# Performance work log

Measured on AMD Instinct MI355X. Metric: run time of the kernel, lower is better.

Reference implementation:

```python
import jax, jax.numpy as jnp
import numpy as np

B, NV, DM, DK, DV, H, DFF = 256, 40, 512, 256, 256, 4, 2048
K1, K2 = 4, 8
EPS = 1e-5


def _knn_mask(vertices, k):
    # square_distance(xyz, xyz): dist[b,i,j] = ||x_i - x_j||^2
    d = -2.0 * jnp.einsum('bic,bjc->bij', vertices, vertices)
    sq = jnp.sum(vertices ** 2, -1)
    d = d + sq[:, :, None] + sq[:, None, :]
    # torch.topk(dist, k, dim=1, largest=False)[1].transpose(1,2) -> [B,N,k]
    idx = jax.lax.top_k(-jnp.swapaxes(d, 1, 2), k)[1]
    counts = jax.nn.one_hot(idx, NV, dtype=jnp.float32).sum(-2)  # [B,N,NV]
    return (counts < 1.0)[:, None, :, :]  # [B,1,N,N], broadcasts over heads (== repeat)


def _ln(x, g, b):
    m = x.mean(-1, keepdims=True)
    v = x.var(-1, keepdims=True)
    return (x - m) / jnp.sqrt(v + EPS) * g + b


def _encoder(x, mask, wq, bq, wk, bk, wv, bv, wo, bo, ln1g, ln1b, w1, b1, w2, b2, ln2g, ln2b):
    Bn, N, _ = x.shape
    q = (x @ wq + bq).reshape(Bn, N, H, DK).transpose(0, 2, 1, 3)   # [B,H,N,DK]
    kk = (x @ wk + bk).reshape(Bn, N, H, DK).transpose(0, 2, 3, 1)  # [B,H,DK,N]
    v = (x @ wv + bv).reshape(Bn, N, H, DV).transpose(0, 2, 1, 3)   # [B,H,N,DV]
    att = jnp.matmul(q, kk) / np.sqrt(DK)                           # [B,H,N,N]
    att = jnp.where(mask, -jnp.inf, att)
    att = jax.nn.softmax(att, axis=-1)
    o = jnp.matmul(att, v).transpose(0, 2, 1, 3).reshape(Bn, N, H * DV) @ wo + bo
    x = _ln(x + o, ln1g, ln1b)                                      # residual + LayerNorm
    ff = jax.nn.relu(x @ w1 + b1) @ w2 + b2                         # position-wise FFN
    return _ln(x + ff, ln2g, ln2b)


def _fusion(y, w1, b1, bng, bnb, w2, b2):
    y = y @ w1 + b1                       # Conv1d(1024,512,1) == per-position linear
    m = y.mean((0, 1))
    v = y.var((0, 1))                     # BatchNorm1d, training-mode batch stats (biased var)
    y = (y - m) / jnp.sqrt(v + EPS) * bng + bnb
    y = jnp.where(y > 0, y, 0.2 * y)      # LeakyReLU(0.2)
    return y @ w2 + b2                    # Conv1d(512,512,1)


def _forward(vertices, F, *p):
    m1 = _knn_mask(vertices, K1)
    m2 = _knn_mask(vertices, K2)
    F1 = _encoder(F, m1, *p[0:16])
    F2 = _encoder(F, m2, *p[16:32])
    yy = jnp.concatenate((F1, F2), -1)    # [B,N,2*DM]
    return _fusion(yy, *p[32:38])


def setup_inputs() -> dict:
    key = jax.random.key(0)
    d = {}
    cnt = [0]
    def nk():
        cnt[0] += 1
        return jax.random.fold_in(key, cnt[0])
    def lin(i, o):
        return jax.random.normal(nk(), (i, o), jnp.float32) * (1.0 / np.sqrt(i))
    d['vertices'] = jax.random.normal(nk(), (B, NV, 3), jnp.float32)
    d['F'] = jax.random.normal(nk(), (B, NV, DM), jnp.float32)
    for pfx in ('e1', 'e2'):
        d[pfx + '_wq'] = lin(DM, H * DK); d[pfx + '_bq'] = jnp.zeros((H * DK,), jnp.float32)
        d[pfx + '_wk'] = lin(DM, H * DK); d[pfx + '_bk'] = jnp.zeros((H * DK,), jnp.float32)
        d[pfx + '_wv'] = lin(DM, H * DV); d[pfx + '_bv'] = jnp.zeros((H * DV,), jnp.float32)
        d[pfx + '_wo'] = lin(H * DV, DM); d[pfx + '_bo'] = jnp.zeros((DM,), jnp.float32)
        d[pfx + '_ln1g'] = jnp.ones((DM,), jnp.float32); d[pfx + '_ln1b'] = jnp.zeros((DM,), jnp.float32)
        d[pfx + '_w1'] = lin(DM, DFF); d[pfx + '_b1'] = jnp.zeros((DFF,), jnp.float32)
        d[pfx + '_w2'] = lin(DFF, DM); d[pfx + '_b2'] = jnp.zeros((DM,), jnp.float32)
        d[pfx + '_ln2g'] = jnp.ones((DM,), jnp.float32); d[pfx + '_ln2b'] = jnp.zeros((DM,), jnp.float32)
    d['fus_w1'] = lin(2 * DM, DM); d['fus_b1'] = jnp.zeros((DM,), jnp.float32)
    d['fus_bng'] = jnp.ones((DM,), jnp.float32); d['fus_bnb'] = jnp.zeros((DM,), jnp.float32)
    d['fus_w2'] = lin(DM, DM); d['fus_b2'] = jnp.zeros((DM,), jnp.float32)
    return d


def reference(vertices, F,
              e1_wq, e1_bq, e1_wk, e1_bk, e1_wv, e1_bv, e1_wo, e1_bo,
              e1_ln1g, e1_ln1b, e1_w1, e1_b1, e1_w2, e1_b2, e1_ln2g, e1_ln2b,
              e2_wq, e2_bq, e2_wk, e2_bk, e2_wv, e2_bv, e2_wo, e2_bo,
              e2_ln1g, e2_ln1b, e2_w1, e2_b1, e2_w2, e2_b2, e2_ln2g, e2_ln2b,
              fus_w1, fus_b1, fus_bng, fus_bnb, fus_w2, fus_b2):
    return _forward(vertices, F,
                    e1_wq, e1_bq, e1_wk, e1_bk, e1_wv, e1_bv, e1_wo, e1_bo,
                    e1_ln1g, e1_ln1b, e1_w1, e1_b1, e1_w2, e1_b2, e1_ln2g, e1_ln2b,
                    e2_wq, e2_bq, e2_wk, e2_bk, e2_wv, e2_bv, e2_wo, e2_bo,
                    e2_ln1g, e2_ln1b, e2_w1, e2_b1, e2_w2, e2_b2, e2_ln2g, e2_ln2b,
                    fus_w1, fus_b1, fus_bng, fus_bnb, fus_w2, fus_b2)
```

## Files before the change

### kernel.cpp

```cpp
#include <hip/hip_runtime.h>

typedef unsigned short u16;
typedef unsigned int   u32;
typedef __attribute__((ext_vector_type(4))) float f32x4;
typedef __attribute__((ext_vector_type(8))) short short8;
typedef __attribute__((ext_vector_type(4))) unsigned short u16x4;

#define DEV __device__ __forceinline__
#define AS1 __attribute__((address_space(1)))
#define AS3 __attribute__((address_space(3)))
#define SB  __builtin_amdgcn_sched_barrier(0)
#define BAR __builtin_amdgcn_s_barrier()

DEV float bf2f(u16 u){ return __uint_as_float(((u32)u)<<16); }
DEV u16 f2bf(float f){ u32 u=__float_as_uint(f); return (u16)((u + 0x7fffu + ((u>>16)&1u))>>16); }
DEV void g2lds16(const void* g, void* l){
  __builtin_amdgcn_global_load_lds((const AS1 void*)g, (AS3 void*)l, 16, 0, 0);
}

struct WtJobs {
  const float* W[14];
  u16*         WT[14];
  int K[14];
  int N[14];
  int off[15];
};

__global__ __launch_bounds__(256) void wtb_kernel(WtJobs J){
  __shared__ u16 tile[32][33];
  int bid = blockIdx.x;
  int j = 0;
  #pragma unroll
  for (int s=1;s<14;++s) if (bid >= J.off[s]) j = s;
  int lb = bid - J.off[j];
  int K = J.K[j], N = J.N[j];
  int nx = N>>5;
  int n0 = (lb % nx)<<5, k0 = (lb / nx)<<5;
  const float* W = J.W[j];
  u16* WT = J.WT[j];
  int tx = threadIdx.x, ty = threadIdx.y;
  #pragma unroll
  for (int i=0;i<4;++i){
    int k = ty + i*8;
    tile[k][tx] = f2bf(W[(size_t)(k0+k)*N + n0 + tx]);
  }
  __syncthreads();
  #pragma unroll
  for (int i=0;i<4;++i){
    int n = ty + i*8;
    WT[(size_t)(n0+n)*K + k0 + tx] = tile[tx][n];
  }
}

__global__ __launch_bounds__(256) void cvt_kernel(const float* __restrict__ in,
                                                  u16* __restrict__ out, long n4){
  long i = ((long)blockIdx.x*256 + threadIdx.x);
  if (i < n4){
    f32x4 v = *(const f32x4*)(in + i*4);
    u16x4 r; r.x=f2bf(v.x); r.y=f2bf(v.y); r.z=f2bf(v.z); r.w=f2bf(v.w);
    *(u16x4*)(out + i*4) = r;
  }
}

__global__ __launch_bounds__(256) void catb_kernel(const float* __restrict__ a,
                                                   const float* __restrict__ b,
                                                   const float* __restrict__ c,
                                                   float* __restrict__ dst){
  int i = blockIdx.x*256 + threadIdx.x;
  if (i < 1024) dst[i] = a[i];
  else if (i < 2048) dst[i] = b[i-1024];
  else if (i < 3072) dst[i] = c[i-2048];
}

__global__ __launch_bounds__(256) void fill_kernel(float* p, float v, long n){
  long i = (long)blockIdx.x*256 + threadIdx.x;
  if (i < n) p[i] = v;
}

__global__ __launch_bounds__(256) void knn_kernel(const float* __restrict__ verts,
                                                  unsigned char* __restrict__ nbr1,
                                                  unsigned char* __restrict__ nbr2){
  __shared__ float P[40][3];
  __shared__ float SQ[40];
  int b = blockIdx.x, tid = threadIdx.x, wave = tid>>6, lane = tid&63;
  if (tid < 40){
    float x = verts[((size_t)b*40+tid)*3+0];
    float y = verts[((size_t)b*40+tid)*3+1];
    float z = verts[((size_t)b*40+tid)*3+2];
    P[tid][0]=x; P[tid][1]=y; P[tid][2]=z;
    SQ[tid] = __fadd_rn(__fadd_rn(__fmul_rn(x,x),__fmul_rn(y,y)),__fmul_rn(z,z));
  }
  __syncthreads();
  for (int i = wave; i < 40; i += 4){
    float d = 3.0e38f;
    if (lane < 40){
      int j = lane;
      float dot = __fadd_rn(__fadd_rn(__fmul_rn(P[i][0],P[j][0]),
                                      __fmul_rn(P[i][1],P[j][1])),
                            __fmul_rn(P[i][2],P[j][2]));
      d = __fadd_rn(__fadd_rn(__fmul_rn(-2.f,dot), SQ[j]), SQ[i]);
    }
    bool taken = false;
    #pragma unroll
    for (int s=0;s<8;++s){
      float v = taken ? 3.0e38f : d;
      float m = v;
      #pragma unroll
      for (int o=32;o;o>>=1) m = fminf(m, __shfl_xor(m, o));
      unsigned long long mask = __ballot(v == m);
      int bj = __ffsll((unsigned long long)mask) - 1;
      if (lane == bj) taken = true;
      if (lane == 0){
        if (s < 4) nbr1[((size_t)b*40+i)*4+s] = (unsigned char)bj;
        nbr2[((size_t)b*40+i)*8+s] = (unsigned char)bj;
      }
    }
  }
}

template<int RELU, int OUTBF>
__global__ __launch_bounds__(256, 4) void gemm_bt(const u16* __restrict__ A,
                                                  const u16* __restrict__ BT,
                                                  const float* __restrict__ bias,
                                                  void* __restrict__ Cout,
                                                  int M, int N, int K){
  __shared__ u16 As[128*32];
  __shared__ u16 Bs[128*32];
  const int tid  = threadIdx.x;
  const int wave = tid>>6, lane = tid&63;
  const int wr = (wave>>1)<<6, wc = (wave&1)<<6;
  const int row0 = blockIdx.x<<7, col0 = blockIdx.y<<7;
  f32x4 acc[4][4];
  #pragma unroll
  for (int i=0;i<4;++i)
    #pragma unroll
    for (int j=0;j<4;++j) acc[i][j] = (f32x4){0.f,0.f,0.f,0.f};

  const int rL = lane>>2;
  const int ch = lane&3;
  const int fr = lane&15, fc = lane>>4;
  const short8* Asv = (const short8*)As;
  const short8* Bsv = (const short8*)Bs;

  for (int kt=0; kt<K; kt+=32){
    #pragma unroll
    for (int c=0;c<2;++c){
      int lo = c*4096 + wave*1024;
      int r  = c*64 + wave*16 + rL;
      int kk = ((ch ^ ((r>>1)&3))<<3);
      g2lds16(A  + (size_t)(row0+r)*K + kt + kk, (char*)As + lo);
      g2lds16(BT + (size_t)(col0+r)*K + kt + kk, (char*)Bs + lo);
    }
    __syncthreads();
    short8 a[4], b[4];
    #pragma unroll
    for (int i=0;i<4;++i){
      int rowA = wr + i*16 + fr;
      int rowB = wc + i*16 + fr;
      a[i] = Asv[rowA*4 + (fc ^ ((rowA>>1)&3))];
      b[i] = Bsv[rowB*4 + (fc ^ ((rowB>>1)&3))];
    }
    #pragma unroll
    for (int i=0;i<4;++i)
      #pragma unroll
      for (int j=0;j<4;++j)
        acc[i][j] = __builtin_amdgcn_mfma_f32_16x16x32_bf16(a[i], b[j], acc[i][j], 0,0,0);
    __syncthreads();
  }
  #pragma unroll
  for (int i=0;i<4;++i){
    int mrow = row0 + wr + i*16 + fc*4;
    #pragma unroll
    for (int j=0;j<4;++j){
      int ncol = col0 + wc + j*16 + fr;
      float bv = bias[ncol];
      #pragma unroll
      for (int r=0;r<4;++r){
        float v = acc[i][j][r] + bv;
        if (RELU) v = v > 0.f ? v : 0.f;
        if (OUTBF) ((u16*)Cout)[(size_t)(mrow+r)*N + ncol] = f2bf(v);
        else       ((float*)Cout)[(size_t)(mrow+r)*N + ncol] = v;
      }
    }
  }
}

DEV void stage32(const u16* __restrict__ gbase, int ldg, u16* __restrict__ buf,
                 int kt, int wave, int lane){
  int srw = wave*16 + (lane>>2);
  int scl = (lane&3) ^ ((srw>>1)&3);
  const u16* src = gbase + (size_t)srw*ldg + kt + scl*8;
  char* dst = (char*)buf + wave*1024;
  g2lds16(src, dst);
  g2lds16(src + (size_t)128*ldg, dst + 8192);
}

template<int RELU>
__global__ __launch_bounds__(512, 1) void gemm256p(const u16* __restrict__ A,
                                                   const u16* __restrict__ BT,
                                                   const float* __restrict__ bias,
                                                   u16* __restrict__ Cout,
                                                   int M, int N, int K){
  __shared__ u16 As[4][256*32];
  __shared__ u16 Bs[4][256*32];
  const int tid  = threadIdx.x;
  const int wave = tid>>6, lane = tid&63;
  const int wm = wave>>2, wn = wave&3;
  const int fr = lane&15, fc = lane>>4;
  const int row0 = blockIdx.x<<8, col0 = blockIdx.y<<8;
  const int NT = K>>5;
  const u16* Ag = A  + (size_t)row0*K;
  const u16* Bg = BT + (size_t)col0*K;

  f32x4 acc[8][4];
  #pragma unroll
  for (int i=0;i<8;++i)
    #pragma unroll
    for (int j=0;j<4;++j) acc[i][j] = (f32x4){0.f,0.f,0.f,0.f};

  stage32(Ag, K, As[0], 0,  wave, lane);  stage32(Bg, K, Bs[0], 0,  wave, lane);
  stage32(Ag, K, As[1], 32, wave, lane);  stage32(Bg, K, Bs[1], 32, wave, lane);
  stage32(Ag, K, As[2], 64, wave, lane);  stage32(Bg, K, Bs[2], 64, wave, lane);
  asm volatile("s_waitcnt vmcnt(8)" ::: "memory");
  SB; BAR; SB;

  for (int t = 0; t < NT; ++t){
    const int cur = t&3, nx3 = (t+3)&3;
    const short8* AV = (const short8*)As[cur];
    const short8* BV = (const short8*)Bs[cur];
    short8 a[4], b[4];
    #pragma unroll
    for (int nf=0;nf<4;++nf){ int rr = wn*64 + nf*16 + fr; b[nf] = BV[rr*4 + (fc ^ ((rr>>1)&3))]; }
    #pragma unroll
    for (int mf=0;mf<4;++mf){ int rr = wm*128 + mf*16 + fr; a[mf] = AV[rr*4 + (fc ^ ((rr>>1)&3))]; }
    if (t+3 < NT) stage32(Ag, K, As[nx3], (t+3)<<5, wave, lane);
    SB; BAR; SB;
    __builtin_amdgcn_s_setprio(1);
    #pragma unroll
    for (int mf=0;mf<4;++mf)
      #pragma unroll
      for (int nf=0;nf<4;++nf)
        acc[mf][nf] = __builtin_amdgcn_mfma_f32_16x16x32_bf16(a[mf], b[nf], acc[mf][nf], 0,0,0);
    __builtin_amdgcn_s_setprio(0);
    SB; BAR; SB;
    #pragma unroll
    for (int mf=0;mf<4;++mf){ int rr = wm*128 + (mf+4)*16 + fr; a[mf] = AV[rr*4 + (fc ^ ((rr>>1)&3))]; }
    if (t+3 < NT) stage32(Bg, K, Bs[nx3], (t+3)<<5, wave, lane);
    {
      int rem = NT - t - 1;
      if (rem >= 3)      asm volatile("s_waitcnt vmcnt(8)" ::: "memory");
      else if (rem == 2) asm volatile("s_waitcnt vmcnt(4)" ::: "memory");
      else if (rem == 1) asm volatile("s_waitcnt vmcnt(0)" ::: "memory");
    }
    SB; BAR; SB;
    __builtin_amdgcn_s_setprio(1);
    #pragma unroll
    for (int mf=0;mf<4;++mf)
      #pragma unroll
      for (int nf=0;nf<4;++nf)
        acc[mf+4][nf] = __builtin_amdgcn_mfma_f32_16x16x32_bf16(a[mf], b[nf], acc[mf+4][nf], 0,0,0);
    __builtin_amdgcn_s_setprio(0);
    SB; BAR; SB;
  }

  #pragma unroll
  for (int i=0;i<8;++i){
    int mrow = row0 + wm*128 + i*16 + fc*4;
    #pragma unroll
    for (int j=0;j<4;++j){
      int ncol = col0 + wn*64 + j*16 + fr;
      float bv = bias[ncol];
      #pragma unroll
      for (int r=0;r<4;++r){
        float v = acc[i][j][r] + bv;
        if (RELU) v = v > 0.f ? v : 0.f;
        Cout[(size_t)(mrow+r)*N + ncol] = f2bf(v);
      }
    }
  }
}

template<int KNB>
__global__ __launch_bounds__(256) void attn_kernel(const u16* __restrict__ QKV,
                                                   const unsigned char* __restrict__ nbr,
                                                   u16* __restrict__ O){
  __shared__ u16 KV[2][40*256];
  int b = blockIdx.x>>2, h = blockIdx.x&3;
  int tid = threadIdx.x, wave = tid>>6, lane = tid&63;
  const size_t rowb = (size_t)b*40;
  for (int c = tid; c < 1280; c += 256){
    int row = c >> 5, col = (c & 31) << 3;
    size_t src = (rowb+row)*3072 + h*256 + col;
    *(short8*)&KV[0][row*256+col] = *(const short8*)(QKV + src + 1024);
    *(short8*)&KV[1][row*256+col] = *(const short8*)(QKV + src + 2048);
  }
  __syncthreads();
  for (int i = wave; i < 40; i += 4){
    int js[KNB];
    if (KNB == 4){
      u32 p = *(const u32*)(nbr + (rowb+i)*4);
      js[0]=p&255; js[1]=(p>>8)&255; js[2]=(p>>16)&255; js[3]=(p>>24)&255;
    } else {
      u32 p0 = *(const u32*)(nbr + (rowb+i)*8);
      u32 p1 = *(const u32*)(nbr + (rowb+i)*8 + 4);
      js[0]=p0&255; js[1]=(p0>>8)&255; js[2]=(p0>>16)&255; js[3]=(p0>>24)&255;
      js[4]=p1&255; js[5]=(p1>>8)&255; js[6]=(p1>>16)&255; js[7]=(p1>>24)&255;
    }
    u16x4 qv = *(const u16x4*)(QKV + (rowb+i)*3072 + h*256 + lane*4);
    float q0=bf2f(qv.x), q1=bf2f(qv.y), q2=bf2f(qv.z), q3=bf2f(qv.w);
    float s[KNB];
    #pragma unroll
    for (int jj=0;jj<KNB;++jj){
      u16x4 kv = *(const u16x4*)&KV[0][js[jj]*256 + lane*4];
      s[jj] = q0*bf2f(kv.x) + q1*bf2f(kv.y) + q2*bf2f(kv.z) + q3*bf2f(kv.w);
    }
    #pragma unroll
    for (int jj=0;jj<KNB;++jj){
      #pragma unroll
      for (int o=32;o;o>>=1) s[jj] += __shfl_xor(s[jj], o);
      s[jj] *= 0.0625f;
    }
    float m = s[0];
    #pragma unroll
    for (int jj=1;jj<KNB;++jj) m = fmaxf(m, s[jj]);
    float sum = 0.f;
    #pragma unroll
    for (int jj=0;jj<KNB;++jj){ s[jj] = expf(s[jj]-m); sum += s[jj]; }
    float inv = 1.f/sum;
    float o0=0.f,o1=0.f,o2=0.f,o3=0.f;
    #pragma unroll
    for (int jj=0;jj<KNB;++jj){
      float w = s[jj]*inv;
      u16x4 vv = *(const u16x4*)&KV[1][js[jj]*256 + lane*4];
      o0 += w*bf2f(vv.x); o1 += w*bf2f(vv.y); o2 += w*bf2f(vv.z); o3 += w*bf2f(vv.w);
    }
    u16x4 r; r.x=f2bf(o0); r.y=f2bf(o1); r.z=f2bf(o2); r.w=f2bf(o3);
    *(u16x4*)(O + (rowb+i)*1024 + h*256 + lane*4) = r;
  }
}

DEV float blockReduce(float v, float* red){
  #pragma unroll
  for (int o=32;o;o>>=1) v += __shfl_xor(v, o);
  int lane = threadIdx.x&63, w = threadIdx.x>>6;
  if (lane==0) red[w] = v;
  __syncthreads();
  float t = red[0]+red[1]+red[2]+red[3];
  __syncthreads();
  return t;
}

__global__ __launch_bounds__(256) void ln_kernel(const float* __restrict__ resf,
                                                 const float* __restrict__ delta,
                                                 const float* __restrict__ g,
                                                 const float* __restrict__ be,
                                                 u16* __restrict__ outb, int ostride, int ocol,
                                                 float* __restrict__ outf){
  __shared__ float red[4];
  int row = blockIdx.x, tid = threadIdx.x;
  size_t ib = (size_t)row*512 + tid*2;
  float2 xr = *(const float2*)(resf+ib);
  float2 xd = *(const float2*)(delta+ib);
  float x0 = xr.x+xd.x, x1 = xr.y+xd.y;
  float s = blockReduce(x0+x1, red);
  float mean = s*(1.f/512.f);
  float d0 = x0-mean, d1 = x1-mean;
  float q = blockReduce(d0*d0+d1*d1, red);
  float inv = 1.f/sqrtf(q*(1.f/512.f)+1e-5f);
  float2 gg = *(const float2*)(g+tid*2);
  float2 bb = *(const float2*)(be+tid*2);
  float r0 = d0*inv*gg.x + bb.x;
  float r1 = d1*inv*gg.y + bb.y;
  size_t ob = (size_t)row*ostride + ocol + tid*2;
  *(u32*)(outb+ob) = ((u32)f2bf(r1)<<16) | (u32)f2bf(r0);
  if (outf){ *(float2*)(outf + ib) = make_float2(r0,r1); }
}

__global__ __launch_bounds__(512) void bn_part(const float* __restrict__ y,
                                               float* __restrict__ psum, float* __restrict__ psq){
  int c = threadIdx.x, blk = blockIdx.x;
  float s = 0.f, q = 0.f;
  for (int r = blk; r < 10240; r += 64){
    float v = y[(size_t)r*512 + c];
    s += v; q += v*v;
  }
  psum[blk*512+c] = s; psq[blk*512+c] = q;
}

__global__ __launch_bounds__(512) void bn_fin(const float* __restrict__ psum,
                                              const float* __restrict__ psq,
                                              const float* __restrict__ g,
                                              const float* __restrict__ b,
                                              float* __restrict__ scale, float* __restrict__ shift){
  int c = threadIdx.x;
  float s = 0.f, q = 0.f;
  for (int k=0;k<64;++k){ s += psum[k*512+c]; q += psq[k*512+c]; }
  float m = s*(1.f/10240.f);
  float var = q*(1.f/10240.f) - m*m;
  float sc = g[c]/sqrtf(var + 1e-5f);
  scale[c] = sc; shift[c] = b[c] - m*sc;
}

__global__ __launch_bounds__(256) void bn_apply(const float* __restrict__ y,
                                                const float* __restrict__ scale,
                                                const float* __restrict__ shift,
                                                u16* __restrict__ out){
  long i4 = ((long)blockIdx.x*256 + threadIdx.x)*4;
  if (i4 < (long)10240*512){
    int c = (int)(i4 & 511);
    f32x4 v  = *(const f32x4*)(y+i4);
    f32x4 sc = *(const f32x4*)(scale+c);
    f32x4 sh = *(const f32x4*)(shift+c);
    f32x4 r;
    #pragma unroll
    for (int k=0;k<4;++k){
      float t = v[k]*sc[k] + sh[k];
      r[k] = t > 0.f ? t : 0.2f*t;
    }
    u16x4 o; o.x=f2bf(r[0]); o.y=f2bf(r[1]); o.z=f2bf(r[2]); o.w=f2bf(r[3]);
    *(u16x4*)(out+i4) = o;
  }
}

extern "C" void kernel_launch(void* const* d_in, const int* in_sizes, int n_in,
                              void* d_out, int out_size, void* d_ws, size_t ws_size,
                              hipStream_t stream){
  const float* verts = (const float*)d_in[0];
  const float* F     = (const float*)d_in[1];
  const float* ew[2][16];
  for (int e=0;e<2;++e) for (int i=0;i<16;++i) ew[e][i] = (const float*)d_in[2+e*16+i];
  const float* fus_w1  = (const float*)d_in[34];
  const float* fus_b1  = (const float*)d_in[35];
  const float* fus_bng = (const float*)d_in[36];
  const float* fus_bnb = (const float*)d_in[37];
  const float* fus_w2  = (const float*)d_in[38];
  const float* fus_b2  = (const float*)d_in[39];

  const int M = 10240;
  size_t off = 0;
  auto alloc = [&](size_t bytes)->void*{
    void* p = (char*)d_ws + off; off = (off + bytes + 255) & ~(size_t)255; return p;
  };
  u16 *wtqkv[2],*wto[2],*wtw1[2],*wtw2[2];
  float* bqkv[2];
  for (int e=0;e<2;++e){
    wtqkv[e] = (u16*)alloc((size_t)3072*512*2);
    wto[e]   = (u16*)alloc((size_t)512*1024*2);
    wtw1[e]  = (u16*)alloc((size_t)2048*512*2);
    wtw2[e]  = (u16*)alloc((size_t)512*2048*2);
    bqkv[e]  = (float*)alloc(3072*4);
  }
  u16*  wtf1 = (u16*)alloc((size_t)512*1024*2);
  u16*  wtf2 = (u16*)alloc((size_t)512*512*2);
  u16*  Fb   = (u16*)alloc((size_t)M*512*2);
  u16*  QKVb = (u16*)alloc((size_t)M*3072*2);
  u16*  H1   = (u16*)alloc((size_t)M*2048*2);
  float* PF  = (float*)alloc((size_t)M*512*4);
  u16*  X1b  = (u16*)alloc((size_t)M*512*2);
  u16*  YC   = (u16*)alloc((size_t)M*1024*2);
  unsigned char* nbr1 = (unsigned char*)alloc(256*40*4);
  unsigned char* nbr2 = (unsigned char*)alloc(256*40*8);
  float* psum = (float*)alloc(64*512*4);
  float* psq  = (float*)alloc(64*512*4);
  float* bnsc = (float*)alloc(512*4);
  float* bnsh = (float*)alloc(512*4);
  u16*   OB  = H1;
  float* X1f = (float*)QKVb;
  float* Y1  = (float*)QKVb;
  u16*   Y2  = (u16*)((char*)QKVb + (size_t)M*512*4);

  if (off > ws_size){
    long n = out_size;
    fill_kernel<<<(unsigned)((n+255)/256),256,0,stream>>>((float*)d_out, 12345.0f, n);
    return;
  }

  WtJobs J;
  int nb = 0, ji = 0;
  auto addjob = [&](const float* W, u16* WT, int K, int N){
    J.W[ji]=W; J.WT[ji]=WT; J.K[ji]=K; J.N[ji]=N; J.off[ji]=nb;
    nb += (N>>5)*(K>>5); ++ji;
  };
  for (int e=0;e<2;++e){
    addjob(ew[e][0],  wtqkv[e],                    512, 1024);
    addjob(ew[e][2],  wtqkv[e]+(size_t)1024*512,   512, 1024);
    addjob(ew[e][4],  wtqkv[e]+(size_t)2048*512,   512, 1024);
    addjob(ew[e][6],  wto[e],  1024, 512);
    addjob(ew[e][10], wtw1[e], 512, 2048);
    addjob(ew[e][12], wtw2[e], 2048, 512);
  }
  addjob(fus_w1, wtf1, 1024, 512);
  addjob(fus_w2, wtf2, 512, 512);
  J.off[14] = nb;
  wtb_kernel<<<nb, dim3(32,8), 0, stream>>>(J);
  for (int e=0;e<2;++e)
    catb_kernel<<<12,256,0,stream>>>(ew[e][1], ew[e][3], ew[e][5], bqkv[e]);
  cvt_kernel<<<5120,256,0,stream>>>(F, Fb, (long)M*512/4);
  knn_kernel<<<256,256,0,stream>>>(verts, nbr1, nbr2);

  for (int e=0;e<2;++e){
    gemm256p<0><<<dim3(40,12),512,0,stream>>>(Fb, wtqkv[e], bqkv[e], QKVb, M, 3072, 512);
    if (e == 0) attn_kernel<4><<<1024,256,0,stream>>>(QKVb, nbr1, OB);
    else        attn_kernel<8><<<1024,256,0,stream>>>(QKVb, nbr2, OB);
    gemm_bt<0,0><<<dim3(80,4),256,0,stream>>>(OB, wto[e], ew[e][7], PF, M, 512, 1024);
    ln_kernel<<<M,256,0,stream>>>(F, PF, ew[e][8], ew[e][9], X1b, 512, 0, X1f);
    gemm256p<1><<<dim3(40,8),512,0,stream>>>(X1b, wtw1[e], ew[e][11], H1, M, 2048, 512);
    gemm_bt<0,0><<<dim3(80,4),256,0,stream>>>(H1, wtw2[e], ew[e][13], PF, M, 512, 2048);
    ln_kernel<<<M,256,0,stream>>>(X1f, PF, ew[e][14], ew[e][15], YC, 1024, e*512, nullptr);
  }

  gemm_bt<0,0><<<dim3(80,4),256,0,stream>>>(YC, wtf1, fus_b1, Y1, M, 512, 1024);
  bn_part<<<64,512,0,stream>>>(Y1, psum, psq);
  bn_fin<<<1,512,0,stream>>>(psum, psq, fus_bng, fus_bnb, bnsc, bnsh);
  bn_apply<<<5120,256,0,stream>>>(Y1, bnsc, bnsh, Y2);
  gemm_bt<0,0><<<dim3(80,4),256,0,stream>>>(Y2, wtf2, fus_b2, d_out, M, 512, 512);
}
```

Baseline: 551.9 us.

## Batch both encoders' post-attention GEMMs and LayerNorms via grid-z dispatch

Runs the QKV GEMM and attention for both encoders first, then processes the O-projection, LN1, FFN1, FFN2 and LN2 of both encoders together in single launches, using blockIdx.z (or y for LN) to select per-encoder pointers with strided layouts. The small 320-block gemm_bt launches become 640 blocks and the FFN1 GEMM grid doubles, which improves GPU fill and halves launch count. Intermediate projection outputs are now stored as bf16 instead of fp32, cutting memory traffic at some precision cost. BatchNorm partial reduction uses 256 blocks instead of 64 for more parallelism. Workspace grows because H1, PF and X1b are widened to hold both encoders.

```diff
diff --git a/kernel.cpp b/kernel.cpp
--- a/kernel.cpp
+++ b/kernel.cpp
@@ -118,12 +118,12 @@
   }
 }
 
+struct GemmZ { const u16* A; const u16* BT; const float* bias; void* C; };
+
 template<int RELU, int OUTBF>
-__global__ __launch_bounds__(256, 4) void gemm_bt(const u16* __restrict__ A,
-                                                  const u16* __restrict__ BT,
-                                                  const float* __restrict__ bias,
-                                                  void* __restrict__ Cout,
-                                                  int M, int N, int K){
+__global__ __launch_bounds__(256, 4) void gemm_btz(GemmZ g0, GemmZ g1,
+                                                   int M, int N, int K, int lda, int ldc){
+  GemmZ g = blockIdx.z ? g1 : g0;
   __shared__ u16 As[128*32];
   __shared__ u16 Bs[128*32];
   const int tid  = threadIdx.x;
@@ -148,8 +148,8 @@
       int lo = c*4096 + wave*1024;
       int r  = c*64 + wave*16 + rL;
       int kk = ((ch ^ ((r>>1)&3))<<3);
-      g2lds16(A  + (size_t)(row0+r)*K + kt + kk, (char*)As + lo);
-      g2lds16(BT + (size_t)(col0+r)*K + kt + kk, (char*)Bs + lo);
+      g2lds16(g.A  + (size_t)(row0+r)*lda + kt + kk, (char*)As + lo);
+      g2lds16(g.BT + (size_t)(col0+r)*K   + kt + kk, (char*)Bs + lo);
     }
     __syncthreads();
     short8 a[4], b[4];
@@ -173,13 +173,13 @@
     #pragma unroll
     for (int j=0;j<4;++j){
       int ncol = col0 + wc + j*16 + fr;
-      float bv = bias[ncol];
+      float bv = g.bias[ncol];
       #pragma unroll
       for (int r=0;r<4;++r){
         float v = acc[i][j][r] + bv;
         if (RELU) v = v > 0.f ? v : 0.f;
-        if (OUTBF) ((u16*)Cout)[(size_t)(mrow+r)*N + ncol] = f2bf(v);
-        else       ((float*)Cout)[(size_t)(mrow+r)*N + ncol] = v;
+        if (OUTBF) ((u16*)g.C)[(size_t)(mrow+r)*ldc + ncol] = f2bf(v);
+        else       ((float*)g.C)[(size_t)(mrow+r)*ldc + ncol] = v;
       }
     }
   }
@@ -196,11 +196,9 @@
 }
 
 template<int RELU>
-__global__ __launch_bounds__(512, 1) void gemm256p(const u16* __restrict__ A,
-                                                   const u16* __restrict__ BT,
-                                                   const float* __restrict__ bias,
-                                                   u16* __restrict__ Cout,
-                                                   int M, int N, int K){
+__global__ __launch_bounds__(512, 1) void gemm256pz(GemmZ g0, GemmZ g1,
+                                                    int M, int N, int K, int lda, int ldc){
+  GemmZ g = blockIdx.z ? g1 : g0;
   __shared__ u16 As[4][256*32];
   __shared__ u16 Bs[4][256*32];
   const int tid  = threadIdx.x;
@@ -209,8 +207,8 @@
   const int fr = lane&15, fc = lane>>4;
   const int row0 = blockIdx.x<<8, col0 = blockIdx.y<<8;
   const int NT = K>>5;
-  const u16* Ag = A  + (size_t)row0*K;
-  const u16* Bg = BT + (size_t)col0*K;
+  const u16* Ag = g.A  + (size_t)row0*lda;
+  const u16* Bg = g.BT + (size_t)col0*K;
 
   f32x4 acc[8][4];
   #pragma unroll
@@ -218,9 +216,9 @@
     #pragma unroll
     for (int j=0;j<4;++j) acc[i][j] = (f32x4){0.f,0.f,0.f,0.f};
 
-  stage32(Ag, K, As[0], 0,  wave, lane);  stage32(Bg, K, Bs[0], 0,  wave, lane);
-  stage32(Ag, K, As[1], 32, wave, lane);  stage32(Bg, K, Bs[1], 32, wave, lane);
-  stage32(Ag, K, As[2], 64, wave, lane);  stage32(Bg, K, Bs[2], 64, wave, lane);
+  stage32(Ag, lda, As[0], 0,  wave, lane);  stage32(Bg, K, Bs[0], 0,  wave, lane);
+  stage32(Ag, lda, As[1], 32, wave, lane);  stage32(Bg, K, Bs[1], 32, wave, lane);
+  stage32(Ag, lda, As[2], 64, wave, lane);  stage32(Bg, K, Bs[2], 64, wave, lane);
   asm volatile("s_waitcnt vmcnt(8)" ::: "memory");
   SB; BAR; SB;
 
@@ -233,7 +231,7 @@
     for (int nf=0;nf<4;++nf){ int rr = wn*64 + nf*16 + fr; b[nf] = BV[rr*4 + (fc ^ ((rr>>1)&3))]; }
     #pragma unroll
     for (int mf=0;mf<4;++mf){ int rr = wm*128 + mf*16 + fr; a[mf] = AV[rr*4 + (fc ^ ((rr>>1)&3))]; }
-    if (t+3 < NT) stage32(Ag, K, As[nx3], (t+3)<<5, wave, lane);
+    if (t+3 < NT) stage32(Ag, lda, As[nx3], (t+3)<<5, wave, lane);
     SB; BAR; SB;
     __builtin_amdgcn_s_setprio(1);
     #pragma unroll
@@ -269,12 +267,12 @@
     #pragma unroll
     for (int j=0;j<4;++j){
       int ncol = col0 + wn*64 + j*16 + fr;
-      float bv = bias[ncol];
+      float bv = g.bias[ncol];
       #pragma unroll
       for (int r=0;r<4;++r){
         float v = acc[i][j][r] + bv;
         if (RELU) v = v > 0.f ? v : 0.f;
-        Cout[(size_t)(mrow+r)*N + ncol] = f2bf(v);
+        ((u16*)g.C)[(size_t)(mrow+r)*ldc + ncol] = f2bf(v);
       }
     }
   }
@@ -283,7 +281,7 @@
 template<int KNB>
 __global__ __launch_bounds__(256) void attn_kernel(const u16* __restrict__ QKV,
                                                    const unsigned char* __restrict__ nbr,
-                                                   u16* __restrict__ O){
+                                                   u16* __restrict__ O, int ldo){
   __shared__ u16 KV[2][40*256];
   int b = blockIdx.x>>2, h = blockIdx.x&3;
   int tid = threadIdx.x, wave = tid>>6, lane = tid&63;
@@ -335,9 +333,12 @@
       o0 += w*bf2f(vv.x); o1 += w*bf2f(vv.y); o2 += w*bf2f(vv.z); o3 += w*bf2f(vv.w);
     }
     u16x4 r; r.x=f2bf(o0); r.y=f2bf(o1); r.z=f2bf(o2); r.w=f2bf(o3);
-    *(u16x4*)(O + (rowb+i)*1024 + h*256 + lane*4) = r;
-  }
-}
+    *(u16x4*)(O + (rowb+i)*(size_t)ldo + h*256 + lane*4) = r;
+  }
+}
+
+struct LnJob { const float* resf; const u16* delta; const float* g; const float* be;
+               u16* outb; float* outf; };
 
 DEV float blockReduce(float v, float* red){
   #pragma unroll
@@ -350,37 +351,34 @@
   return t;
 }
 
-__global__ __launch_bounds__(256) void ln_kernel(const float* __restrict__ resf,
-                                                 const float* __restrict__ delta,
-                                                 const float* __restrict__ g,
-                                                 const float* __restrict__ be,
-                                                 u16* __restrict__ outb, int ostride, int ocol,
-                                                 float* __restrict__ outf){
+__global__ __launch_bounds__(256) void ln2_kernel(LnJob j0, LnJob j1, int rstride){
   __shared__ float red[4];
+  LnJob j = blockIdx.y ? j1 : j0;
   int row = blockIdx.x, tid = threadIdx.x;
-  size_t ib = (size_t)row*512 + tid*2;
-  float2 xr = *(const float2*)(resf+ib);
-  float2 xd = *(const float2*)(delta+ib);
-  float x0 = xr.x+xd.x, x1 = xr.y+xd.y;
+  size_t ibr = (size_t)row*rstride + tid*2;
+  size_t ibd = (size_t)row*1024 + tid*2;
+  float2 xr = *(const float2*)(j.resf+ibr);
+  u32 dp = *(const u32*)(j.delta+ibd);
+  float x0 = xr.x + bf2f((u16)(dp&0xffffu));
+  float x1 = xr.y + bf2f((u16)(dp>>16));
   float s = blockReduce(x0+x1, red);
   float mean = s*(1.f/512.f);
   float d0 = x0-mean, d1 = x1-mean;
   float q = blockReduce(d0*d0+d1*d1, red);
   float inv = 1.f/sqrtf(q*(1.f/512.f)+1e-5f);
-  float2 gg = *(const float2*)(g+tid*2);
-  float2 bb = *(const float2*)(be+tid*2);
+  float2 gg = *(const float2*)(j.g+tid*2);
+  float2 bb = *(const float2*)(j.be+tid*2);
   float r0 = d0*inv*gg.x + bb.x;
   float r1 = d1*inv*gg.y + bb.y;
-  size_t ob = (size_t)row*ostride + ocol + tid*2;
-  *(u32*)(outb+ob) = ((u32)f2bf(r1)<<16) | (u32)f2bf(r0);
-  if (outf){ *(float2*)(outf + ib) = make_float2(r0,r1); }
+  *(u32*)(j.outb + ibd) = ((u32)f2bf(r1)<<16) | (u32)f2bf(r0);
+  if (j.outf) *(float2*)(j.outf + ibd) = make_float2(r0,r1);
 }
 
 __global__ __launch_bounds__(512) void bn_part(const float* __restrict__ y,
                                                float* __restrict__ psum, float* __restrict__ psq){
   int c = threadIdx.x, blk = blockIdx.x;
   float s = 0.f, q = 0.f;
-  for (int r = blk; r < 10240; r += 64){
+  for (int r = blk; r < 10240; r += 256){
     float v = y[(size_t)r*512 + c];
     s += v; q += v*v;
   }
@@ -394,7 +392,7 @@
                                               float* __restrict__ scale, float* __restrict__ shift){
   int c = threadIdx.x;
   float s = 0.f, q = 0.f;
-  for (int k=0;k<64;++k){ s += psum[k*512+c]; q += psq[k*512+c]; }
+  for (int k=0;k<256;++k){ s += psum[k*512+c]; q += psq[k*512+c]; }
   float m = s*(1.f/10240.f);
   float var = q*(1.f/10240.f) - m*m;
   float sc = g[c]/sqrtf(var + 1e-5f);
@@ -454,20 +452,20 @@
   u16*  wtf2 = (u16*)alloc((size_t)512*512*2);
   u16*  Fb   = (u16*)alloc((size_t)M*512*2);
   u16*  QKVb = (u16*)alloc((size_t)M*3072*2);
-  u16*  H1   = (u16*)alloc((size_t)M*2048*2);
-  float* PF  = (float*)alloc((size_t)M*512*4);
-  u16*  X1b  = (u16*)alloc((size_t)M*512*2);
+  u16*  H1   = (u16*)alloc((size_t)M*4096*2);
+  u16*  PF   = (u16*)alloc((size_t)M*1024*2);
+  u16*  X1b  = (u16*)alloc((size_t)M*1024*2);
   u16*  YC   = (u16*)alloc((size_t)M*1024*2);
   unsigned char* nbr1 = (unsigned char*)alloc(256*40*4);
   unsigned char* nbr2 = (unsigned char*)alloc(256*40*8);
-  float* psum = (float*)alloc(64*512*4);
-  float* psq  = (float*)alloc(64*512*4);
+  float* psum = (float*)alloc(256*512*4);
+  float* psq  = (float*)alloc(256*512*4);
   float* bnsc = (float*)alloc(512*4);
   float* bnsh = (float*)alloc(512*4);
   u16*   OB  = H1;
   float* X1f = (float*)QKVb;
   float* Y1  = (float*)QKVb;
-  u16*   Y2  = (u16*)((char*)QKVb + (size_t)M*512*4);
+  u16*   Y2  = (u16*)((char*)QKVb + (size_t)24*1024*1024);
 
   if (off > ws_size){
     long n = out_size;
@@ -499,19 +497,47 @@
   knn_kernel<<<256,256,0,stream>>>(verts, nbr1, nbr2);
 
   for (int e=0;e<2;++e){
-    gemm256p<0><<<dim3(40,12),512,0,stream>>>(Fb, wtqkv[e], bqkv[e], QKVb, M, 3072, 512);
-    if (e == 0) attn_kernel<4><<<1024,256,0,stream>>>(QKVb, nbr1, OB);
-    else        attn_kernel<8><<<1024,256,0,stream>>>(QKVb, nbr2, OB);
-    gemm_bt<0,0><<<dim3(80,4),256,0,stream>>>(OB, wto[e], ew[e][7], PF, M, 512, 1024);
-    ln_kernel<<<M,256,0,stream>>>(F, PF, ew[e][8], ew[e][9], X1b, 512, 0, X1f);
-    gemm256p<1><<<dim3(40,8),512,0,stream>>>(X1b, wtw1[e], ew[e][11], H1, M, 2048, 512);
-    gemm_bt<0,0><<<dim3(80,4),256,0,stream>>>(H1, wtw2[e], ew[e][13], PF, M, 512, 2048);
-    ln_kernel<<<M,256,0,stream>>>(X1f, PF, ew[e][14], ew[e][15], YC, 1024, e*512, nullptr);
-  }
-
-  gemm_bt<0,0><<<dim3(80,4),256,0,stream>>>(YC, wtf1, fus_b1, Y1, M, 512, 1024);
-  bn_part<<<64,512,0,stream>>>(Y1, psum, psq);
+    GemmZ q{Fb, wtqkv[e], bqkv[e], QKVb};
+    gemm256pz<0><<<dim3(40,12,1),512,0,stream>>>(q, q, M, 3072, 512, 512, 3072);
+    if (e == 0) attn_kernel<4><<<1024,256,0,stream>>>(QKVb, nbr1, OB,        2048);
+    else        attn_kernel<8><<<1024,256,0,stream>>>(QKVb, nbr2, OB + 1024, 2048);
+  }
+
+  {
+    GemmZ o0{OB,        wto[0], ew[0][7], PF};
+    GemmZ o1{OB + 1024, wto[1], ew[1][7], PF + 512};
+    gemm_btz<0,1><<<dim3(80,4,2),256,0,stream>>>(o0, o1, M, 512, 1024, 2048, 1024);
+  }
+  {
+    LnJob a{F, PF,       ew[0][8], ew[0][9], X1b,       X1f};
+    LnJob b{F, PF + 512, ew[1][8], ew[1][9], X1b + 512, X1f + 512};
+    ln2_kernel<<<dim3(M,2),256,0,stream>>>(a, b, 512);
+  }
+  {
+    GemmZ f0{X1b,       wtw1[0], ew[0][11], H1};
+    GemmZ f1{X1b + 512, wtw1[1], ew[1][11], H1 + 2048};
+    gemm256pz<1><<<dim3(40,8,2),512,0,stream>>>(f0, f1, M, 2048, 512, 1024, 4096);
+  }
+  {
+    GemmZ f0{H1,        wtw2[0], ew[0][13], PF};
+    GemmZ f1{H1 + 2048, wtw2[1], ew[1][13], PF + 512};
+    gemm_btz<0,1><<<dim3(80,4,2),256,0,stream>>>(f0, f1, M, 512, 2048, 4096, 1024);
+  }
+  {
+    LnJob a{X1f,       PF,       ew[0][14], ew[0][15], YC,       nullptr};
+    LnJob b{X1f + 512, PF + 512, ew[1][14], ew[1][15], YC + 512, nullptr};
+    ln2_kernel<<<dim3(M,2),256,0,stream>>>(a, b, 1024);
+  }
+
+  {
+    GemmZ fz{YC, wtf1, fus_b1, Y1};
+    gemm_btz<0,0><<<dim3(80,4,1),256,0,stream>>>(fz, fz, M, 512, 1024, 1024, 512);
+  }
+  bn_part<<<256,512,0,stream>>>(Y1, psum, psq);
   bn_fin<<<1,512,0,stream>>>(psum, psq, fus_bng, fus_bnb, bnsc, bnsh);
   bn_apply<<<5120,256,0,stream>>>(Y1, bnsc, bnsh, Y2);
-  gemm_bt<0,0><<<dim3(80,4),256,0,stream>>>(Y2, wtf2, fus_b2, d_out, M, 512, 512);
-}
+  {
+    GemmZ fz{Y2, wtf2, fus_b2, d_out};
+    gemm_btz<0,0><<<dim3(80,4,1),256,0,stream>>>(fz, fz, M, 512, 512, 512, 512);
+  }
+}
```

Result: faster. 461.4 us (-16.4%).
